# Optimization experiments

Hardware: AMD Instinct MI355X
Metric: run time of the kernel (lower is better)

The kernel has to match this reference:

```python
import jax, jax.numpy as jnp
import numpy as np

B, S, D, E, TOP_K = 2, 1024, 1024, 8, 2
H = 4 * D  # FFN hidden


def setup_inputs() -> dict:
    key = jax.random.key(0)
    ks = jax.random.split(key, 12)
    sc = 0.02
    return {
        "x": jax.random.normal(ks[0], (B, S, D), jnp.float32),
        # gate: nn.Linear(D, E) -> weight [E, D], bias [E]; routing bias param [E]
        "Wg": jax.random.normal(ks[1], (E, D), jnp.float32) * sc,
        "bg": jnp.zeros((E,), jnp.float32),
        "bias": jnp.zeros((E,), jnp.float32),
        # routed experts: stacked Linear(D,4D) and Linear(4D,D) weights (torch layout [out,in])
        "W1": jax.random.normal(ks[2], (E, H, D), jnp.float32) * sc,
        "b1": jnp.zeros((E, H), jnp.float32),
        "W2": jax.random.normal(ks[3], (E, D, H), jnp.float32) * sc,
        "b2": jnp.zeros((E, D), jnp.float32),
        # shared expert
        "Ws1": jax.random.normal(ks[4], (H, D), jnp.float32) * sc,
        "bs1": jnp.zeros((H,), jnp.float32),
        "Ws2": jax.random.normal(ks[5], (D, H), jnp.float32) * sc,
        "bs2": jnp.zeros((D,), jnp.float32),
    }


def reference(x, Wg, bg, bias, W1, b1, W2, b2, Ws1, bs1, Ws2, bs2):
    b, s, d = x.shape
    xf = x.reshape(-1, d)  # [T, D]
    T = xf.shape[0]

    # sigmoid gating with learnable routing bias
    scores = jax.nn.sigmoid(xf @ Wg.T + bg + bias)          # [T, E]
    top_scores, top_idx = jax.lax.top_k(scores, TOP_K)      # [T, K]

    # per-token per-expert combine weights (zero for unselected experts)
    weights = jnp.zeros((T, E), scores.dtype)
    weights = weights.at[jnp.arange(T)[:, None], top_idx].add(top_scores)  # [T, E]

    # dense grouped expert MLP (mask-and-matmul form of gather-GEMM-scatter)
    h = jax.nn.gelu(jnp.einsum("td,ehd->teh", xf, W1) + b1, approximate=False)  # [T, E, H]
    eo = jnp.einsum("teh,edh->ted", h, W2) + b2                                  # [T, E, D]
    combined = jnp.einsum("ted,te->td", eo, weights)                             # [T, D]

    # shared expert applied to every token
    shared = jax.nn.gelu(xf @ Ws1.T + bs1, approximate=False) @ Ws2.T + bs2      # [T, D]

    return (shared + combined).reshape(b, s, d)
```

## Files before the change

### kernel.cpp

```cpp
#include <hip/hip_runtime.h>
#include <hip/hip_bf16.h>
#include <math.h>

#define NTOK 2048
#define DDIM 1024
#define HDIM 4096
#define NEXP 8
#define NROWS (3 * NTOK)
#define KSPLIT2 2

typedef __bf16 bf16x8 __attribute__((ext_vector_type(8)));
typedef float f32x4 __attribute__((ext_vector_type(4)));
typedef __attribute__((address_space(1))) char as1_char;
typedef __attribute__((address_space(3))) char as3_char;

__device__ __forceinline__ void async16(const void* g, void* l) {
  __builtin_amdgcn_global_load_lds((as1_char*)g, (as3_char*)l, 16, 0, 0);
}

__device__ __forceinline__ float gelu_fast(float v) {
  const float x = v * 0.70710678118654752f;
  const float ax = fabsf(x);
  const float t = __builtin_amdgcn_rcpf(1.0f + 0.3275911f * ax);
  float p = 1.061405429f;
  p = p * t - 1.453152027f;
  p = p * t + 1.421413741f;
  p = p * t - 0.284496736f;
  p = p * t + 0.254829592f;
  const float y = 1.0f - p * t * __expf(-ax * ax);
  const float erfv = copysignf(y, x);
  return 0.5f * v * (1.0f + erfv);
}

__global__ void moe_zero_misc(int* counts) {
  if (threadIdx.x < NEXP) counts[threadIdx.x] = 0;
}

__device__ __forceinline__ void cvt2048(const float* __restrict__ src,
                                        __hip_bfloat16* __restrict__ dst,
                                        int tid) {
  const size_t i = (size_t)tid * 8;
  const float4 a = *(const float4*)(src + i);
  const float4 b = *(const float4*)(src + i + 4);
  union { __hip_bfloat16 h[8]; uint4 u; } p;
  p.h[0] = __float2bfloat16(a.x); p.h[1] = __float2bfloat16(a.y);
  p.h[2] = __float2bfloat16(a.z); p.h[3] = __float2bfloat16(a.w);
  p.h[4] = __float2bfloat16(b.x); p.h[5] = __float2bfloat16(b.y);
  p.h[6] = __float2bfloat16(b.z); p.h[7] = __float2bfloat16(b.w);
  *(uint4*)(dst + i) = p.u;
}

__global__ void __launch_bounds__(256) moe_pre(
    const float* __restrict__ x, const float* __restrict__ Wg,
    const float* __restrict__ bg, const float* __restrict__ bias,
    const float* __restrict__ W1, const float* __restrict__ Ws1,
    __hip_bfloat16* __restrict__ xbf, __hip_bfloat16* __restrict__ W1bf,
    __hip_bfloat16* __restrict__ Ws1bf, float* __restrict__ out,
    int* __restrict__ counts, int* __restrict__ topk_idx,
    float* __restrict__ topk_w, int* __restrict__ slot) {
  const int b = blockIdx.x, tid = threadIdx.x;
  if (b < 512) {
    const int t = b * 4 + (tid >> 6);
    const int lane = tid & 63;
    float xv[16];
#pragma unroll
    for (int q = 0; q < 16; ++q) xv[q] = x[(size_t)t * DDIM + q * 64 + lane];
    float sc[NEXP];
#pragma unroll
    for (int e = 0; e < NEXP; ++e) {
      float s = 0.f;
#pragma unroll
      for (int q = 0; q < 16; ++q) s += xv[q] * Wg[(size_t)e * DDIM + q * 64 + lane];
#pragma unroll
      for (int o = 32; o > 0; o >>= 1) s += __shfl_xor(s, o, 64);
      sc[e] = 1.0f / (1.0f + expf(-(s + bg[e] + bias[e])));
    }
    if (lane == 0) {
      int k0 = 0;
      for (int e = 1; e < NEXP; ++e)
        if (sc[e] > sc[k0]) k0 = e;
      int k1 = (k0 == 0) ? 1 : 0;
      for (int e = 0; e < NEXP; ++e) {
        if (e == k0) continue;
        if (sc[e] > sc[k1]) k1 = e;
      }
      topk_idx[t * 2 + 0] = k0;
      topk_idx[t * 2 + 1] = k1;
      topk_w[t * 2 + 0] = sc[k0];
      topk_w[t * 2 + 1] = sc[k1];
      slot[t * 2 + 0] = atomicAdd(&counts[k0], 1);
      slot[t * 2 + 1] = atomicAdd(&counts[k1], 1);
    }
    return;
  }
  const int cb = b - 512;
  if (cb < 1024) { cvt2048(x + (size_t)cb * 2048, xbf + (size_t)cb * 2048, tid); return; }
  if (cb < 17408) { const size_t o = (size_t)(cb - 1024) * 2048; cvt2048(W1 + o, W1bf + o, tid); return; }
  if (cb < 19456) { const size_t o = (size_t)(cb - 17408) * 2048; cvt2048(Ws1 + o, Ws1bf + o, tid); return; }
  const size_t o = (size_t)(cb - 19456) * 2048 + (size_t)tid * 8;
  *(float4*)(out + o) = make_float4(0.f, 0.f, 0.f, 0.f);
  *(float4*)(out + o + 4) = make_float4(0.f, 0.f, 0.f, 0.f);
}

__device__ __forceinline__ void gemm_core(const char* const ga[4], const char* const gb[4],
                                          char* sm, int Kbytes, int tid,
                                          f32x4 acc[4][4]) {
  const int w = tid >> 6, l = tid & 63;
  const int lr = l & 15, quad = l >> 4;
  const int wr = w >> 1, wc = w & 1;
  const int s8 = lr & 7;
  const int slot0 = (quad ^ s8) * 16;
  const int slot1 = ((4 + quad) ^ s8) * 16;
  const int abase = (wr * 64 + lr) * 128;
  const int bbase = 16384 + (wc * 64 + lr) * 128;
  const int niter = Kbytes >> 7;

  auto stage = [&](int it, int buf) {
    char* base = sm + buf * 32768;
    const int kb = it * 128;
#pragma unroll
    for (int q = 0; q < 4; ++q) {
      async16(ga[q] + kb, base + w * 4096 + q * 1024);
      async16(gb[q] + kb, base + 16384 + w * 4096 + q * 1024);
    }
  };

  stage(0, 0);
  for (int i = 0; i < niter; ++i) {
    const int cur = i & 1;
    if (i + 1 < niter) {
      stage(i + 1, cur ^ 1);
      __builtin_amdgcn_s_waitcnt(0x0F78);
    } else {
      __builtin_amdgcn_s_waitcnt(0x0F70);
    }
    __builtin_amdgcn_s_barrier();
    const char* rb = sm + cur * 32768;
    bf16x8 av[4][2], bv[4][2];
#pragma unroll
    for (int i2 = 0; i2 < 4; ++i2) {
      av[i2][0] = *(const bf16x8*)(rb + abase + i2 * 2048 + slot0);
      av[i2][1] = *(const bf16x8*)(rb + abase + i2 * 2048 + slot1);
    }
#pragma unroll
    for (int j = 0; j < 4; ++j) {
      bv[j][0] = *(const bf16x8*)(rb + bbase + j * 2048 + slot0);
      bv[j][1] = *(const bf16x8*)(rb + bbase + j * 2048 + slot1);
    }
#pragma unroll
    for (int s = 0; s < 2; ++s)
#pragma unroll
      for (int i2 = 0; i2 < 4; ++i2)
#pragma unroll
        for (int j = 0; j < 4; ++j)
          acc[i2][j] = __builtin_amdgcn_mfma_f32_16x16x32_bf16(av[i2][s], bv[j][s], acc[i2][j], 0, 0, 0);
    __builtin_amdgcn_s_barrier();
  }
}

__device__ __forceinline__ void xcd_decode(int hw, int& g, int& m) {
  m = (hw >> 3) & 7;
  g = (hw & 7) + 8 * (hw >> 6);
}

__global__ void moe_scan(const int* __restrict__ counts, int* __restrict__ offsets) {
  if (threadIdx.x == 0) {
    int s = 0;
    for (int e = 0; e < NEXP; ++e) { offsets[e] = s; s += counts[e]; }
    offsets[NEXP] = s;
  }
}

__global__ void moe_scatter(const int* __restrict__ topk_idx, const float* __restrict__ topk_w,
                            const int* __restrict__ slot, const int* __restrict__ offsets,
                            int* __restrict__ row_token, float* __restrict__ row_w) {
  const int t = blockIdx.x * blockDim.x + threadIdx.x;
  if (t >= NTOK) return;
#pragma unroll
  for (int k = 0; k < 2; ++k) {
    const int e = topk_idx[t * 2 + k];
    const int rg = offsets[e] + slot[t * 2 + k];
    row_token[rg] = t;
    row_w[rg] = topk_w[t * 2 + k];
  }
  row_token[2 * NTOK + t] = t;
  row_w[2 * NTOK + t] = 1.0f;
}

__device__ __forceinline__ void cvt_w2_quota(int b, const float* __restrict__ W2,
                                             const float* __restrict__ Ws2,
                                             __hip_bfloat16* __restrict__ W2bf,
                                             __hip_bfloat16* __restrict__ Ws2bf,
                                             int tid) {
  const float* src;
  __hip_bfloat16* dst;
  size_t base;
  if (b < 4096) { src = W2; dst = W2bf; base = (size_t)b * 8192; }
  else          { src = Ws2; dst = Ws2bf; base = (size_t)(b - 4096) * 8192; }
#pragma unroll
  for (int k = 0; k < 8; ++k) {
    const size_t i = base + (size_t)k * 1024 + (size_t)tid * 4;
    const float4 a = *(const float4*)(src + i);
    union { __hip_bfloat16 h[4]; uint2 u; } p;
    p.h[0] = __float2bfloat16(a.x); p.h[1] = __float2bfloat16(a.y);
    p.h[2] = __float2bfloat16(a.z); p.h[3] = __float2bfloat16(a.w);
    *(uint2*)(dst + i) = p.u;
  }
}

__global__ void __launch_bounds__(256) moe_gemm1(
    const __hip_bfloat16* __restrict__ xbf, const __hip_bfloat16* __restrict__ W1bf,
    const float* __restrict__ b1, const __hip_bfloat16* __restrict__ Ws1bf,
    const float* __restrict__ bs1, const int* __restrict__ counts,
    const int* __restrict__ offsets, const int* __restrict__ row_token,
    __hip_bfloat16* __restrict__ h1, const float* __restrict__ W2,
    const float* __restrict__ Ws2, __hip_bfloat16* __restrict__ W2bf,
    __hip_bfloat16* __restrict__ Ws2bf) {
  __shared__ alignas(16) char sm[65536];
  const int tid = threadIdx.x;
  int g, m;
  xcd_decode(blockIdx.x, g, m);
  const int nt = m + 8 * (g & 3);
  const int mt = (g >> 2) & 15;
  const int e = g >> 6;
  const int cnt = (e < NEXP) ? counts[e] : NTOK;
  if (mt * 128 >= cnt) {
    cvt_w2_quota(blockIdx.x, W2, Ws2, W2bf, Ws2bf, tid);
    return;
  }
  const int off = (e < NEXP) ? offsets[e] : 2 * NTOK;
  const __hip_bfloat16* Bw = (e < NEXP) ? (W1bf + (size_t)e * HDIM * DDIM) : Ws1bf;
  const float* bb = (e < NEXP) ? (b1 + e * HDIM) : bs1;

  const int w = tid >> 6, l = tid & 63;
  const int rl8 = l >> 3;
  const int cg = ((l & 7) ^ rl8) * 16;

  const char* ga[4];
  const char* gb[4];
#pragma unroll
  for (int q = 0; q < 4; ++q) {
    const int r = mt * 128 + w * 32 + q * 8 + rl8;
    const int c = (r < cnt) ? r : (cnt - 1);
    const int tok = row_token[off + c];
    ga[q] = (const char*)xbf + (size_t)tok * (DDIM * 2) + cg;
    gb[q] = (const char*)Bw + (size_t)(nt * 128 + w * 32 + q * 8 + rl8) * (DDIM * 2) + cg;
  }

  f32x4 acc[4][4] = {};
  gemm_core(ga, gb, sm, DDIM * 2, tid, acc);

  const int lr = l & 15, quad = l >> 4, wr = w >> 1, wc = w & 1;
#pragma unroll
  for (int i = 0; i < 4; ++i) {
#pragma unroll
    for (int r = 0; r < 4; ++r) {
      const int rowe = mt * 128 + wr * 64 + i * 16 + quad * 4 + r;
      if (rowe >= cnt) continue;
      const size_t orow = (size_t)(off + rowe) * HDIM;
#pragma unroll
      for (int j = 0; j < 4; ++j) {
        const int h = nt * 128 + wc * 64 + j * 16 + lr;
        const float v = acc[i][j][r] + bb[h];
        h1[orow + h] = __float2bfloat16(gelu_fast(v));
      }
    }
  }
  cvt_w2_quota(blockIdx.x, W2, Ws2, W2bf, Ws2bf, tid);
}

__global__ void __launch_bounds__(256) moe_gemm2(
    const __hip_bfloat16* __restrict__ h1, const __hip_bfloat16* __restrict__ W2bf,
    const float* __restrict__ b2, const __hip_bfloat16* __restrict__ Ws2bf,
    const float* __restrict__ bs2, const int* __restrict__ counts,
    const int* __restrict__ offsets, const int* __restrict__ row_token,
    const float* __restrict__ row_w, float* __restrict__ out) {
  __shared__ alignas(16) char sm[65536];
  int g, m;
  xcd_decode(blockIdx.x, g, m);
  const int nt = m;
  const int kc = g & 1;
  const int mt = (g >> 1) & 15;
  const int e = g >> 5;
  const int cnt = (e < NEXP) ? counts[e] : NTOK;
  if (mt * 128 >= cnt) return;
  const int off = (e < NEXP) ? offsets[e] : 2 * NTOK;
  const __hip_bfloat16* Bw = (e < NEXP) ? (W2bf + (size_t)e * DDIM * HDIM) : Ws2bf;
  const float* bb = (e < NEXP) ? (b2 + e * DDIM) : bs2;

  const int tid = threadIdx.x;
  const int w = tid >> 6, l = tid & 63;
  const int rl8 = l >> 3;
  const int cg = ((l & 7) ^ rl8) * 16;
  const int KB = (HDIM * 2) / KSPLIT2;
  const size_t kofs = (size_t)kc * KB;

  const char* ga[4];
  const char* gb[4];
#pragma unroll
  for (int q = 0; q < 4; ++q) {
    const int ar = mt * 128 + w * 32 + q * 8 + rl8;
    ga[q] = (const char*)h1 + (size_t)(off + ar) * (HDIM * 2) + kofs + cg;
    gb[q] = (const char*)Bw + (size_t)(nt * 128 + w * 32 + q * 8 + rl8) * (HDIM * 2) + kofs + cg;
  }

  f32x4 acc[4][4] = {};
  gemm_core(ga, gb, sm, KB, tid, acc);

  const int lr = l & 15, quad = l >> 4, wr = w >> 1, wc = w & 1;
#pragma unroll
  for (int i = 0; i < 4; ++i) {
#pragma unroll
    for (int r = 0; r < 4; ++r) {
      const int rowe = mt * 128 + wr * 64 + i * 16 + quad * 4 + r;
      if (rowe >= cnt) continue;
      const int rg = off + rowe;
      const int tok = row_token[rg];
      const float wt = row_w[rg];
#pragma unroll
      for (int j = 0; j < 4; ++j) {
        const int d = nt * 128 + wc * 64 + j * 16 + lr;
        const float base = (kc == 0) ? bb[d] : 0.f;
        atomicAdd(&out[(size_t)tok * DDIM + d], wt * (acc[i][j][r] + base));
      }
    }
  }
}

extern "C" void kernel_launch(void* const* d_in, const int* in_sizes, int n_in,
                              void* d_out, int out_size, void* d_ws, size_t ws_size,
                              hipStream_t stream) {
  (void)in_sizes; (void)n_in; (void)out_size; (void)ws_size;
  const float* x    = (const float*)d_in[0];
  const float* Wg   = (const float*)d_in[1];
  const float* bg   = (const float*)d_in[2];
  const float* bias = (const float*)d_in[3];
  const float* W1   = (const float*)d_in[4];
  const float* b1   = (const float*)d_in[5];
  const float* W2   = (const float*)d_in[6];
  const float* b2   = (const float*)d_in[7];
  const float* Ws1  = (const float*)d_in[8];
  const float* bs1  = (const float*)d_in[9];
  const float* Ws2  = (const float*)d_in[10];
  const float* bs2  = (const float*)d_in[11];
  float* out = (float*)d_out;

  char* ws = (char*)d_ws;
  size_t cur = 0;
  auto take = [&](size_t b) -> void* {
    void* p = ws + cur;
    cur += (b + 255) & ~(size_t)255;
    return p;
  };
  int* counts    = (int*)take(NEXP * 4);
  int* offsets   = (int*)take((NEXP + 1) * 4);
  int* topk_idx  = (int*)take(NTOK * 2 * 4);
  float* topk_w  = (float*)take(NTOK * 2 * 4);
  int* slot      = (int*)take(NTOK * 2 * 4);
  int* row_token = (int*)take(NROWS * 4);
  float* row_w   = (float*)take(NROWS * 4);
  __hip_bfloat16* xbf   = (__hip_bfloat16*)take((size_t)NTOK * DDIM * 2);
  __hip_bfloat16* W1bf  = (__hip_bfloat16*)take((size_t)NEXP * HDIM * DDIM * 2);
  __hip_bfloat16* W2bf  = (__hip_bfloat16*)take((size_t)NEXP * DDIM * HDIM * 2);
  __hip_bfloat16* Ws1bf = (__hip_bfloat16*)take((size_t)HDIM * DDIM * 2);
  __hip_bfloat16* Ws2bf = (__hip_bfloat16*)take((size_t)DDIM * HDIM * 2);
  __hip_bfloat16* h1    = (__hip_bfloat16*)take((size_t)(NROWS + 64) * HDIM * 2);

  moe_zero_misc<<<1, 64, 0, stream>>>(counts);

  moe_pre<<<20992, 256, 0, stream>>>(x, Wg, bg, bias, W1, Ws1,
                                     xbf, W1bf, Ws1bf, out,
                                     counts, topk_idx, topk_w, slot);

  moe_scan<<<1, 1, 0, stream>>>(counts, offsets);
  moe_scatter<<<NTOK / 256, 256, 0, stream>>>(topk_idx, topk_w, slot, offsets, row_token, row_w);

  moe_gemm1<<<4608, 256, 0, stream>>>(xbf, W1bf, b1, Ws1bf, bs1, counts, offsets,
                                      row_token, h1, W2, Ws2, W2bf, Ws2bf);

  moe_gemm2<<<2304, 256, 0, stream>>>(h1, W2bf, b2, Ws2bf, bs2, counts, offsets,
                                      row_token, row_w, out);
}
```

Baseline: 328.2 us.

## Drop scan kernel by computing expert offsets inline; use 128x64 tiles in GEMM2

Removes the separate single-thread prefix-scan launch and the offsets buffer. Each consumer now sums the expert counts inline to get its row offset, which saves one serial kernel launch. GEMM2 switches from 128x128 to 128x64 output tiles with a dedicated core and smaller LDS, doubling the grid to 4608 blocks. This should give better occupancy and load balance over the ragged expert tiles, at the cost of less reuse of A per block and more atomic traffic blocks.

After: 314.0 us. 4.3% less time.

```diff
diff --git a/kernel.cpp b/kernel.cpp
--- a/kernel.cpp
+++ b/kernel.cpp
@@ -34,6 +34,13 @@
 
 __global__ void moe_zero_misc(int* counts) {
   if (threadIdx.x < NEXP) counts[threadIdx.x] = 0;
+}
+
+__device__ __forceinline__ int off_of(const int* __restrict__ counts, int e) {
+  if (e >= NEXP) return 2 * NTOK;
+  int s = 0;
+  for (int i = 0; i < e; ++i) s += counts[i];
+  return s;
 }
 
 __device__ __forceinline__ void cvt2048(const float* __restrict__ src,
@@ -158,28 +165,78 @@
   }
 }
 
+__device__ __forceinline__ void gemm2_core(const char* const ga[4], const char* const gb[2],
+                                           char* sm, int Kbytes, int tid,
+                                           f32x4 acc[4][2]) {
+  const int w = tid >> 6, l = tid & 63;
+  const int lr = l & 15, quad = l >> 4;
+  const int wr = w >> 1, wc = w & 1;
+  const int s8 = lr & 7;
+  const int slot0 = (quad ^ s8) * 16;
+  const int slot1 = ((4 + quad) ^ s8) * 16;
+  const int abase = (wr * 64 + lr) * 128;
+  const int bbase = 16384 + (wc * 32 + lr) * 128;
+  const int niter = Kbytes >> 7;
+
+  auto stage = [&](int it, int buf) {
+    char* base = sm + buf * 24576;
+    const int kb = it * 128;
+#pragma unroll
+    for (int q = 0; q < 4; ++q)
+      async16(ga[q] + kb, base + w * 4096 + q * 1024);
+#pragma unroll
+    for (int q = 0; q < 2; ++q)
+      async16(gb[q] + kb, base + 16384 + w * 2048 + q * 1024);
+  };
+
+  stage(0, 0);
+  for (int i = 0; i < niter; ++i) {
+    const int cur = i & 1;
+    if (i + 1 < niter) {
+      stage(i + 1, cur ^ 1);
+      __builtin_amdgcn_s_waitcnt(0x0F76);
+    } else {
+      __builtin_amdgcn_s_waitcnt(0x0F70);
+    }
+    __builtin_amdgcn_s_barrier();
+    const char* rb = sm + cur * 24576;
+    bf16x8 av[4][2], bv[2][2];
+#pragma unroll
+    for (int i2 = 0; i2 < 4; ++i2) {
+      av[i2][0] = *(const bf16x8*)(rb + abase + i2 * 2048 + slot0);
+      av[i2][1] = *(const bf16x8*)(rb + abase + i2 * 2048 + slot1);
+    }
+#pragma unroll
+    for (int j = 0; j < 2; ++j) {
+      bv[j][0] = *(const bf16x8*)(rb + bbase + j * 2048 + slot0);
+      bv[j][1] = *(const bf16x8*)(rb + bbase + j * 2048 + slot1);
+    }
+#pragma unroll
+    for (int s = 0; s < 2; ++s)
+#pragma unroll
+      for (int i2 = 0; i2 < 4; ++i2)
+#pragma unroll
+        for (int j = 0; j < 2; ++j)
+          acc[i2][j] = __builtin_amdgcn_mfma_f32_16x16x32_bf16(av[i2][s], bv[j][s], acc[i2][j], 0, 0, 0);
+    __builtin_amdgcn_s_barrier();
+  }
+}
+
 __device__ __forceinline__ void xcd_decode(int hw, int& g, int& m) {
   m = (hw >> 3) & 7;
   g = (hw & 7) + 8 * (hw >> 6);
 }
 
-__global__ void moe_scan(const int* __restrict__ counts, int* __restrict__ offsets) {
-  if (threadIdx.x == 0) {
-    int s = 0;
-    for (int e = 0; e < NEXP; ++e) { offsets[e] = s; s += counts[e]; }
-    offsets[NEXP] = s;
-  }
-}
-
-__global__ void moe_scatter(const int* __restrict__ topk_idx, const float* __restrict__ topk_w,
-                            const int* __restrict__ slot, const int* __restrict__ offsets,
+__global__ void moe_scatter(const int* __restrict__ counts,
+                            const int* __restrict__ topk_idx, const float* __restrict__ topk_w,
+                            const int* __restrict__ slot,
                             int* __restrict__ row_token, float* __restrict__ row_w) {
   const int t = blockIdx.x * blockDim.x + threadIdx.x;
   if (t >= NTOK) return;
 #pragma unroll
   for (int k = 0; k < 2; ++k) {
     const int e = topk_idx[t * 2 + k];
-    const int rg = offsets[e] + slot[t * 2 + k];
+    const int rg = off_of(counts, e) + slot[t * 2 + k];
     row_token[rg] = t;
     row_w[rg] = topk_w[t * 2 + k];
   }
@@ -212,7 +269,7 @@
     const __hip_bfloat16* __restrict__ xbf, const __hip_bfloat16* __restrict__ W1bf,
     const float* __restrict__ b1, const __hip_bfloat16* __restrict__ Ws1bf,
     const float* __restrict__ bs1, const int* __restrict__ counts,
-    const int* __restrict__ offsets, const int* __restrict__ row_token,
+    const int* __restrict__ row_token,
     __hip_bfloat16* __restrict__ h1, const float* __restrict__ W2,
     const float* __restrict__ Ws2, __hip_bfloat16* __restrict__ W2bf,
     __hip_bfloat16* __restrict__ Ws2bf) {
@@ -228,7 +285,7 @@
     cvt_w2_quota(blockIdx.x, W2, Ws2, W2bf, Ws2bf, tid);
     return;
   }
-  const int off = (e < NEXP) ? offsets[e] : 2 * NTOK;
+  const int off = off_of(counts, e);
   const __hip_bfloat16* Bw = (e < NEXP) ? (W1bf + (size_t)e * HDIM * DDIM) : Ws1bf;
   const float* bb = (e < NEXP) ? (b1 + e * HDIM) : bs1;
 
@@ -273,18 +330,18 @@
     const __hip_bfloat16* __restrict__ h1, const __hip_bfloat16* __restrict__ W2bf,
     const float* __restrict__ b2, const __hip_bfloat16* __restrict__ Ws2bf,
     const float* __restrict__ bs2, const int* __restrict__ counts,
-    const int* __restrict__ offsets, const int* __restrict__ row_token,
+    const int* __restrict__ row_token,
     const float* __restrict__ row_w, float* __restrict__ out) {
-  __shared__ alignas(16) char sm[65536];
+  __shared__ alignas(16) char sm[49152];
   int g, m;
   xcd_decode(blockIdx.x, g, m);
-  const int nt = m;
-  const int kc = g & 1;
-  const int mt = (g >> 1) & 15;
-  const int e = g >> 5;
+  const int nt = m + 8 * (g & 1);
+  const int kc = (g >> 1) & 1;
+  const int mt = (g >> 2) & 15;
+  const int e = g >> 6;
   const int cnt = (e < NEXP) ? counts[e] : NTOK;
   if (mt * 128 >= cnt) return;
-  const int off = (e < NEXP) ? offsets[e] : 2 * NTOK;
+  const int off = off_of(counts, e);
   const __hip_bfloat16* Bw = (e < NEXP) ? (W2bf + (size_t)e * DDIM * HDIM) : Ws2bf;
   const float* bb = (e < NEXP) ? (b2 + e * DDIM) : bs2;
 
@@ -296,16 +353,20 @@
   const size_t kofs = (size_t)kc * KB;
 
   const char* ga[4];
-  const char* gb[4];
+  const char* gb[2];
 #pragma unroll
   for (int q = 0; q < 4; ++q) {
     const int ar = mt * 128 + w * 32 + q * 8 + rl8;
     ga[q] = (const char*)h1 + (size_t)(off + ar) * (HDIM * 2) + kofs + cg;
-    gb[q] = (const char*)Bw + (size_t)(nt * 128 + w * 32 + q * 8 + rl8) * (HDIM * 2) + kofs + cg;
-  }
-
-  f32x4 acc[4][4] = {};
-  gemm_core(ga, gb, sm, KB, tid, acc);
+  }
+#pragma unroll
+  for (int q = 0; q < 2; ++q) {
+    const int br = nt * 64 + w * 16 + q * 8 + rl8;
+    gb[q] = (const char*)Bw + (size_t)br * (HDIM * 2) + kofs + cg;
+  }
+
+  f32x4 acc[4][2] = {};
+  gemm2_core(ga, gb, sm, KB, tid, acc);
 
   const int lr = l & 15, quad = l >> 4, wr = w >> 1, wc = w & 1;
 #pragma unroll
@@ -318,8 +379,8 @@
       const int tok = row_token[rg];
       const float wt = row_w[rg];
 #pragma unroll
-      for (int j = 0; j < 4; ++j) {
-        const int d = nt * 128 + wc * 64 + j * 16 + lr;
+      for (int j = 0; j < 2; ++j) {
+        const int d = nt * 64 + wc * 32 + j * 16 + lr;
         const float base = (kc == 0) ? bb[d] : 0.f;
         atomicAdd(&out[(size_t)tok * DDIM + d], wt * (acc[i][j][r] + base));
       }
@@ -353,7 +414,6 @@
     return p;
   };
   int* counts    = (int*)take(NEXP * 4);
-  int* offsets   = (int*)take((NEXP + 1) * 4);
   int* topk_idx  = (int*)take(NTOK * 2 * 4);
   float* topk_w  = (float*)take(NTOK * 2 * 4);
   int* slot      = (int*)take(NTOK * 2 * 4);
@@ -372,12 +432,12 @@
                                      xbf, W1bf, Ws1bf, out,
                                      counts, topk_idx, topk_w, slot);
 
-  moe_scan<<<1, 1, 0, stream>>>(counts, offsets);
-  moe_scatter<<<NTOK / 256, 256, 0, stream>>>(topk_idx, topk_w, slot, offsets, row_token, row_w);
-
-  moe_gemm1<<<4608, 256, 0, stream>>>(xbf, W1bf, b1, Ws1bf, bs1, counts, offsets,
+  moe_scatter<<<NTOK / 256, 256, 0, stream>>>(counts, topk_idx, topk_w, slot,
+                                              row_token, row_w);
+
+  moe_gemm1<<<4608, 256, 0, stream>>>(xbf, W1bf, b1, Ws1bf, bs1, counts,
                                       row_token, h1, W2, Ws2, W2bf, Ws2bf);
 
-  moe_gemm2<<<2304, 256, 0, stream>>>(h1, W2bf, b2, Ws2bf, bs2, counts, offsets,
+  moe_gemm2<<<4608, 256, 0, stream>>>(h1, W2bf, b2, Ws2bf, bs2, counts,
                                       row_token, row_w, out);
 }
```
